# Kernel tuning notes

Hardware: AMD Instinct MI355X
Metric: run time of the kernel (lower is better)

## Reference

```python
import jax, jax.numpy as jnp
import numpy as np

# ---- static configuration (mirrors ConvolutionConfig) ----
B_IMG, C_IN, H, W = 8, 16, 32, 32
C_OUT = 64
KH, KW = 5, 5          # receptive_field
SH, SW = 2, 2          # stride
PH, PW = 2, 2          # padding
N_BITS = 6             # n_inputs_per_node
HIDDEN = [36, 6, 1]    # 6^2, 6^1, 6^0 (tree_depth=2)
INPUT_SIZE = C_IN * KH * KW  # 400
OH = (H + 2 * PH - KH) // SH + 1  # 16
OW = (W + 2 * PW - KW) // SW + 1  # 16


def setup_inputs() -> dict:
    key = jax.random.key(0)
    ks = jax.random.split(key, 7)
    x = jax.random.uniform(ks[0], (B_IMG, C_IN, H, W), dtype=jnp.float32)
    # per-tree random input mappings (6 inputs per LUT node)
    idx0 = jax.random.randint(ks[1], (C_OUT, HIDDEN[0], N_BITS), 0, INPUT_SIZE)
    idx1 = jax.random.randint(ks[2], (C_OUT, HIDDEN[1], N_BITS), 0, HIDDEN[0])
    idx2 = jax.random.randint(ks[3], (C_OUT, HIDDEN[2], N_BITS), 0, HIDDEN[1])
    # raw LUT tables (64 entries), passed through sigmoid in forward
    table0 = jax.random.normal(ks[4], (C_OUT, HIDDEN[0], 64), dtype=jnp.float32)
    table1 = jax.random.normal(ks[5], (C_OUT, HIDDEN[1], 64), dtype=jnp.float32)
    table2 = jax.random.normal(ks[6], (C_OUT, HIDDEN[2], 64), dtype=jnp.float32)
    return {"x": x, "idx0": idx0, "table0": table0, "idx1": idx1,
            "table1": table1, "idx2": idx2, "table2": table2}


def _unfold(x):
    """torch nn.Unfold equivalent -> rows of [B*L, C*KH*KW], c slowest."""
    xp = jnp.pad(x, ((0, 0), (0, 0), (PH, PH), (PW, PW)))
    ri = (jnp.arange(OH) * SH)[:, None] + jnp.arange(KH)[None, :]  # [OH,KH]
    ci = (jnp.arange(OW) * SW)[:, None] + jnp.arange(KW)[None, :]  # [OW,KW]
    # [B, C, OH, OW, KH, KW]
    p = xp[:, :, ri[:, None, :, None], ci[None, :, None, :]]
    p = jnp.transpose(p, (0, 2, 3, 1, 4, 5))  # [B, OH, OW, C, KH, KW]
    return p.reshape(B_IMG * OH * OW, INPUT_SIZE)


def _lut_nodes(g, table):
    """Differentiable LUT node (multilinear interpolation over 2^6 table).
    g: [B, T, N, 6] probabilistic bits in [0,1]; table: [T, N, 64].
    Output: [B, T, N] = sum_a sigmoid(table)[a] * prod_i (g_i if bit_i(a) else 1-g_i).
    Computed by sequential bit contraction to avoid a [B,T,N,64] product tensor.
    """
    T, N = table.shape[0], table.shape[1]
    f = jnp.stack([1.0 - g, g], axis=-1)  # [B,T,N,6,2]
    w = jax.nn.sigmoid(table)             # [T,N,64]
    # contract most-significant bit first
    acc = jnp.einsum('tnkr,btnk->btnr', w.reshape(T, N, 2, 32), f[..., 0, :])
    for b in range(1, N_BITS):
        acc = jnp.einsum('btnkr,btnk->btnr',
                         acc.reshape(acc.shape[0], T, N, 2, -1), f[..., b, :])
    return acc[..., 0]  # [B,T,N]


def reference(x, idx0, table0, idx1, table1, idx2, table2):
    p = _unfold(x)                       # [BP, 400], BP = B*OH*OW
    tind = jnp.arange(C_OUT)[:, None, None]
    # first layer (chunked in torch; mathematically one big gathered layer)
    g0 = p[:, idx0]                      # [BP, C_OUT, 36, 6]
    h0 = _lut_nodes(g0, table0)          # [BP, C_OUT, 36]
    # tree layer 1: 36 -> 6 per tree
    g1 = h0[:, tind, idx1]               # [BP, C_OUT, 6, 6]
    h1 = _lut_nodes(g1, table1)          # [BP, C_OUT, 6]
    # tree layer 2: 6 -> 1 per tree
    g2 = h1[:, tind, idx2]               # [BP, C_OUT, 1, 6]
    h2 = _lut_nodes(g2, table2)[..., 0]  # [BP, C_OUT]
    out = h2.reshape(B_IMG, OH * OW, C_OUT)
    out = jnp.transpose(out, (0, 2, 1)).reshape(B_IMG, C_OUT, OH, OW)
    return out
```

## Files before the change

### kernel.cpp

```cpp
#include <hip/hip_runtime.h>

#define B_IMG 8
#define C_IN  16
#define COUT  64
#define H0    36
#define H1    6
#define NB    6
#define NNODE 43

typedef float f32x2 __attribute__((ext_vector_type(2)));

__device__ __forceinline__ float sigf(float v) { return 1.0f / (1.0f + __expf(-v)); }

__device__ __forceinline__ float lut_contract_reg(const float4 lo4[8], const float4 dd4[8],
                                                  const float g[NB]) {
    f32x2 v[16];
    const float g0 = g[0];
#pragma unroll
    for (int q = 0; q < 8; ++q) {
        v[2*q+0] = (f32x2){lo4[q].x, lo4[q].y} + (f32x2){dd4[q].x, dd4[q].y} * g0;
        v[2*q+1] = (f32x2){lo4[q].z, lo4[q].w} + (f32x2){dd4[q].z, dd4[q].w} * g0;
    }
#pragma unroll
    for (int i = 1; i < 5; ++i) {
        const int vh = 16 >> i;
        const float gi = g[i];
#pragma unroll
        for (int r = 0; r < vh; ++r)
            v[r] += (v[r + vh] - v[r]) * gi;
    }
    return v[0].x + (v[0].y - v[0].x) * g[5];
}

__device__ __forceinline__ void load_tbl_lds(const float* tb, float4 lo4[8], float4 dd4[8]) {
    const float4* t4 = (const float4*)tb;
#pragma unroll
    for (int q = 0; q < 8; ++q) { lo4[q] = t4[q]; dd4[q] = t4[q + 8]; }
}

__global__ __launch_bounds__(512, 4) void lutone_kernel(
    const float* __restrict__ x,
    const int*   __restrict__ idx0,
    const float* __restrict__ t0,
    const int*   __restrict__ idx1,
    const float* __restrict__ t1,
    const int*   __restrict__ idx2,
    const float* __restrict__ t2,
    float*       __restrict__ out)
{
    __shared__ float tblL[NNODE*64];
    __shared__ float h0s[H0*256];
    __shared__ float h1s[H1*256];

    const int tid  = threadIdx.x;
    const int w    = tid >> 6;
    const int lane = tid & 63;
    const int t    = blockIdx.x & 63;
    const int img  = blockIdx.x >> 6;

    for (int e = tid; e < NNODE*32; e += 512) {
        const int node = e >> 5, k = e & 31;
        const float* src = (node < H0)      ? t0 + ((size_t)t*H0 + node)*64
                         : (node < H0+H1)   ? t1 + ((size_t)t*H1 + node - H0)*64
                                            : t2 + (size_t)t*64;
        const float lo = sigf(src[k]);
        const float hi = sigf(src[k + 32]);
        tblL[node*64 + k]      = lo;
        tblL[node*64 + 32 + k] = hi - lo;
    }

    const int* i1base = idx1 + t*(H1*NB);
    unsigned long long umask = 0ull;
#pragma unroll
    for (int j = 0; j < H1*NB; ++j) umask |= 1ull << i1base[j];

    int base[4], vmask[4];
#pragma unroll
    for (int c = 0; c < 4; ++c) {
        const int p  = (c << 6) + lane;
        const int oh = p >> 4, ow = p & 15;
        base[c] = img*16384 + oh*64 + ow*2;
        const int hm = 0x1F ^ ((oh == 0) ? 0x03 : 0) ^ ((oh == 15) ? 0x10 : 0);
        const int wm = 0x1F ^ ((ow == 0) ? 0x03 : 0) ^ ((ow == 15) ? 0x10 : 0);
        int vm = 0;
#pragma unroll
        for (int kh = 0; kh < 5; ++kh)
            vm |= ((hm >> kh) & 1) ? (wm << (5*kh)) : 0;
        vmask[c] = vm;
    }
    __syncthreads();

    int cnt = 0;
    for (int n = 0; n < H0; ++n) {
        if (!((umask >> n) & 1ull)) continue;
        const int slot = cnt++;
        if ((slot & 7) != w) continue;

        const int* i0 = idx0 + ((size_t)t*H0 + n)*NB;
        int off[NB], rem[NB];
#pragma unroll
        for (int i = 0; i < NB; ++i) {
            const int raw = i0[i];
            const int c2  = raw / 25;
            rem[i] = raw - 25*c2;
            const int kh = rem[i] / 5, kw = rem[i] - 5*kh;
            off[i] = c2*1024 + kh*32 + kw - 66;
        }
        float4 lo4[8], dd4[8];
        load_tbl_lds(tblL + n*64, lo4, dd4);
#pragma unroll
        for (int c = 0; c < 4; ++c) {
            float g[NB];
#pragma unroll
            for (int i = 0; i < NB; ++i) {
                const bool ok = ((vmask[c] >> rem[i]) & 1) != 0;
                const float v = x[ok ? (base[c] + off[i]) : 0];
                g[i] = ok ? v : 0.0f;
            }
            h0s[n*256 + (c << 6) + lane] = lut_contract_reg(lo4, dd4, g);
        }
    }
    __syncthreads();

    if (w < H1) {
        float4 lo4[8], dd4[8];
        load_tbl_lds(tblL + (H0 + w)*64, lo4, dd4);
        const int* i1 = idx1 + ((size_t)t*H1 + w)*NB;
        const int s0 = i1[0], s1 = i1[1], s2 = i1[2];
        const int s3 = i1[3], s4 = i1[4], s5 = i1[5];
#pragma unroll
        for (int c = 0; c < 4; ++c) {
            const int px = (c << 6) + lane;
            float g[NB];
            g[0] = h0s[s0*256 + px]; g[1] = h0s[s1*256 + px]; g[2] = h0s[s2*256 + px];
            g[3] = h0s[s3*256 + px]; g[4] = h0s[s4*256 + px]; g[5] = h0s[s5*256 + px];
            h1s[w*256 + px] = lut_contract_reg(lo4, dd4, g);
        }
    }
    __syncthreads();

    if (w < 4) {
        float4 lo4[8], dd4[8];
        load_tbl_lds(tblL + (H0 + H1)*64, lo4, dd4);
        const int* i2 = idx2 + (size_t)t*NB;
        const int px = (w << 6) + lane;
        float g[NB];
#pragma unroll
        for (int i = 0; i < NB; ++i) g[i] = h1s[i2[i]*256 + px];
        out[((size_t)img*COUT + t)*256 + px] = lut_contract_reg(lo4, dd4, g);
    }
}

extern "C" void kernel_launch(void* const* d_in, const int* in_sizes, int n_in,
                              void* d_out, int out_size, void* d_ws, size_t ws_size,
                              hipStream_t stream) {
    const float* x      = (const float*)d_in[0];
    const int*   idx0   = (const int*)  d_in[1];
    const float* table0 = (const float*)d_in[2];
    const int*   idx1   = (const int*)  d_in[3];
    const float* table1 = (const float*)d_in[4];
    const int*   idx2   = (const int*)  d_in[5];
    const float* table2 = (const float*)d_in[6];
    float* out = (float*)d_out;

    lutone_kernel<<<COUT * B_IMG, 512, 0, stream>>>(
        x, idx0, table0, idx1, table1, idx2, table2, out);
}
```

Measured before the change: 21.83 us.

## Precompute idx0 offsets in LDS, unroll node assignment, rebalance layer-1 work

The idx0 decoding (division by 25 and 5) moves into a cooperative LDS prefill, so each node's offsets arrive as three int4 LDS reads instead of per-warp global loads and integer divides. The dynamic per-warp node loop becomes up to five statically unrolled node slots, which lets the compiler schedule loads across nodes at the cost of more code and registers. Layer-1 work is rebalanced so warps 6 and 7, previously idle, handle the last pixel chunk for three nodes each while warps 0-5 do three chunks instead of four.

New measurement: 21.68 us. Within noise of the previous version (-0.7%).

```diff
diff --git a/kernel.cpp b/kernel.cpp
--- a/kernel.cpp
+++ b/kernel.cpp
@@ -51,6 +51,7 @@
     __shared__ float tblL[NNODE*64];
     __shared__ float h0s[H0*256];
     __shared__ float h1s[H1*256];
+    __shared__ int   metaL[H0*NB*2];
 
     const int tid  = threadIdx.x;
     const int w    = tid >> 6;
@@ -68,6 +69,14 @@
         tblL[node*64 + k]      = lo;
         tblL[node*64 + 32 + k] = hi - lo;
     }
+    if (tid < H0*NB) {
+        const int raw = idx0[(size_t)t*(H0*NB) + tid];
+        const int c2  = raw / 25;
+        const int rem = raw - 25*c2;
+        const int kh  = rem / 5, kw = rem - 5*kh;
+        metaL[tid*2 + 0] = c2*1024 + kh*32 + kw - 66;
+        metaL[tid*2 + 1] = rem;
+    }
 
     const int* i1base = idx1 + t*(H1*NB);
     unsigned long long umask = 0ull;
@@ -88,38 +97,50 @@
             vm |= ((hm >> kh) & 1) ? (wm << (5*kh)) : 0;
         vmask[c] = vm;
     }
+
+    int myn0 = -1, myn1 = -1, myn2 = -1, myn3 = -1, myn4 = -1;
+    {
+        int cnt = 0;
+        for (int n = 0; n < H0; ++n) {
+            if (!((umask >> n) & 1ull)) continue;
+            const int slot = cnt++;
+            if ((slot & 7) != w) continue;
+            const int k = slot >> 3;
+            if      (k == 0) myn0 = n;
+            else if (k == 1) myn1 = n;
+            else if (k == 2) myn2 = n;
+            else if (k == 3) myn3 = n;
+            else             myn4 = n;
+        }
+    }
     __syncthreads();
 
-    int cnt = 0;
-    for (int n = 0; n < H0; ++n) {
-        if (!((umask >> n) & 1ull)) continue;
-        const int slot = cnt++;
-        if ((slot & 7) != w) continue;
-
-        const int* i0 = idx0 + ((size_t)t*H0 + n)*NB;
-        int off[NB], rem[NB];
-#pragma unroll
-        for (int i = 0; i < NB; ++i) {
-            const int raw = i0[i];
-            const int c2  = raw / 25;
-            rem[i] = raw - 25*c2;
-            const int kh = rem[i] / 5, kw = rem[i] - 5*kh;
-            off[i] = c2*1024 + kh*32 + kw - 66;
-        }
-        float4 lo4[8], dd4[8];
-        load_tbl_lds(tblL + n*64, lo4, dd4);
-#pragma unroll
-        for (int c = 0; c < 4; ++c) {
-            float g[NB];
-#pragma unroll
-            for (int i = 0; i < NB; ++i) {
-                const bool ok = ((vmask[c] >> rem[i]) & 1) != 0;
-                const float v = x[ok ? (base[c] + off[i]) : 0];
-                g[i] = ok ? v : 0.0f;
-            }
-            h0s[n*256 + (c << 6) + lane] = lut_contract_reg(lo4, dd4, g);
-        }
-    }
+#define NODE_A(NN)                                                           \
+    if ((NN) >= 0) {                                                         \
+        const int4* mp = (const int4*)(metaL + (NN)*12);                     \
+        const int4 ma = mp[0], mb = mp[1], mc = mp[2];                       \
+        float4 lo4[8], dd4[8];                                               \
+        load_tbl_lds(tblL + (NN)*64, lo4, dd4);                              \
+        _Pragma("unroll")                                                    \
+        for (int c = 0; c < 4; ++c) {                                        \
+            const int off_[NB] = {ma.x, ma.z, mb.x, mb.z, mc.x, mc.z};       \
+            const int rem_[NB] = {ma.y, ma.w, mb.y, mb.w, mc.y, mc.w};       \
+            float g[NB];                                                     \
+            _Pragma("unroll")                                                \
+            for (int i = 0; i < NB; ++i) {                                   \
+                const bool ok = ((vmask[c] >> rem_[i]) & 1) != 0;            \
+                const float v = x[ok ? (base[c] + off_[i]) : 0];             \
+                g[i] = ok ? v : 0.0f;                                        \
+            }                                                                \
+            h0s[(NN)*256 + (c << 6) + lane] = lut_contract_reg(lo4, dd4, g); \
+        }                                                                    \
+    }
+    NODE_A(myn0)
+    NODE_A(myn1)
+    NODE_A(myn2)
+    NODE_A(myn3)
+    NODE_A(myn4)
+#undef NODE_A
     __syncthreads();
 
     if (w < H1) {
@@ -129,12 +150,27 @@
         const int s0 = i1[0], s1 = i1[1], s2 = i1[2];
         const int s3 = i1[3], s4 = i1[4], s5 = i1[5];
 #pragma unroll
-        for (int c = 0; c < 4; ++c) {
+        for (int c = 0; c < 3; ++c) {
             const int px = (c << 6) + lane;
             float g[NB];
             g[0] = h0s[s0*256 + px]; g[1] = h0s[s1*256 + px]; g[2] = h0s[s2*256 + px];
             g[3] = h0s[s3*256 + px]; g[4] = h0s[s4*256 + px]; g[5] = h0s[s5*256 + px];
             h1s[w*256 + px] = lut_contract_reg(lo4, dd4, g);
+        }
+    } else {
+        const int nb0 = (w == 6) ? 0 : 3;
+        const int px  = (3 << 6) + lane;
+#pragma unroll
+        for (int k = 0; k < 3; ++k) {
+            const int n = nb0 + k;
+            float4 lo4[8], dd4[8];
+            load_tbl_lds(tblL + (H0 + n)*64, lo4, dd4);
+            const int* i1 = idx1 + ((size_t)t*H1 + n)*NB;
+            float g[NB];
+            g[0] = h0s[i1[0]*256 + px]; g[1] = h0s[i1[1]*256 + px];
+            g[2] = h0s[i1[2]*256 + px]; g[3] = h0s[i1[3]*256 + px];
+            g[4] = h0s[i1[4]*256 + px]; g[5] = h0s[i1[5]*256 + px];
+            h1s[n*256 + px] = lut_contract_reg(lo4, dd4, g);
         }
     }
     __syncthreads();
```
